# Performance work log

Measured on AMD Instinct MI355X. Metric: run time of the kernel, lower is better.

The kernel has to match this reference:

```python
import jax, jax.numpy as jnp
import numpy as np

H = 4          # num_heads (= num_kv_heads, num_kv_groups = 1)
DK = 256       # head_k_dim
DV = 256       # head_v_dim
M = 256        # num_slots
GATE_NORM = 16.0
EPS = 1e-5


def _rmsnorm(x, w):
    var = jnp.mean(jnp.square(x), axis=-1, keepdims=True)
    return x * jax.lax.rsqrt(var + EPS) * w


def _swish(x):
    return x * jax.nn.sigmoid(x)


def setup_inputs() -> dict:
    key = jax.random.key(0)
    ks = jax.random.split(key, 8)
    B, T, D = 4, 2048, 1024
    scale = 2 ** (-2.5) * (2.0 / (D + D)) ** 0.5 * (3.0 ** 0.5) * 2  # ~xavier*gain magnitude
    return {
        "hidden_states": jax.random.normal(ks[0], (B, T, D), jnp.float32),
        "norm_weight": jnp.ones((D,), jnp.float32),
        "w_q": jax.random.normal(ks[1], (D, D), jnp.float32) * scale,
        "w_k": jax.random.normal(ks[2], (D, D), jnp.float32) * scale,
        "w_v": jax.random.normal(ks[3], (D, D), jnp.float32) * scale,
        "w_f": jax.random.normal(ks[4], (H * M, D), jnp.float32) * scale,
        "gnorm_weight": jnp.ones((D,), jnp.float32),
        "w_o": jax.random.normal(ks[5], (D, D), jnp.float32) * scale,
    }


def _gsa_scan(q, k, v, s, g):
    # all inputs time-major: q [T,B,H,DK], k [T,B,H,DK], v [T,B,H,DV],
    # s [T,B,H,M] (slot write strength), g [T,B,H,M] (log forget gate)
    B, Hh = q.shape[1], q.shape[2]
    Hk0 = jnp.zeros((B, Hh, DK, M), q.dtype)
    Hv0 = jnp.zeros((B, Hh, M, DV), q.dtype)

    def step(carry, xs):
        Hk, Hv = carry
        qt, kt, vt, st, gt = xs
        lam = jnp.exp(gt)                                       # [B,H,M]
        # pass 1: linear attn over slots (gate on value/slot dim)
        Hk = Hk * lam[:, :, None, :] + kt[..., :, None] * st[..., None, :]
        z = jnp.einsum('bhk,bhkm->bhm', qt, Hk)                 # slot logits
        p = jax.nn.softmax(z, axis=-1)                          # slot read weights
        # pass 2: linear attn from slots to values (gate on key/slot dim)
        Hv = Hv * lam[..., :, None] + st[..., :, None] * vt[..., None, :]
        ot = jnp.einsum('bhm,bhmv->bhv', p, Hv)
        return (Hk, Hv), ot

    _, o = jax.lax.scan(step, (Hk0, Hv0), (q, k, v, s, g))
    return o  # [T,B,H,DV]


def reference(hidden_states, norm_weight, w_q, w_k, w_v, w_f, gnorm_weight, w_o):
    B, T, D = hidden_states.shape
    h = _rmsnorm(hidden_states, norm_weight)                    # norm_first
    q = _swish(h @ w_q.T).reshape(B, T, H, DK)                  # swish feature map
    k = _swish(h @ w_k.T).reshape(B, T, H, DK)
    v = _swish(h @ w_v.T).reshape(B, T, H, DV)
    f = jax.nn.log_sigmoid(h @ w_f.T).reshape(B, T, H, M) / GATE_NORM
    s = 1.0 - jnp.exp(f)
    tm = lambda x: jnp.transpose(x, (1, 0, 2, 3))               # [B,T,H,*] -> [T,B,H,*]
    o = _gsa_scan(tm(q), tm(k), tm(v), tm(s), tm(f))            # [T,B,H,DV]
    o = jnp.transpose(o, (1, 0, 2, 3)).reshape(B, T, H * DV)
    # use_norm & no output gate: swish -> RMSNorm -> o_proj
    o = _swish(o)
    o = _rmsnorm(o, gnorm_weight)
    return o @ w_o.T
```

## Files before the change

kernel.cpp:

```cpp
#include <hip/hip_runtime.h>
#include <hip/hip_bf16.h>

typedef unsigned short u16;
typedef unsigned int u32;

using bf16x8 = __bf16 __attribute__((ext_vector_type(8)));
using s16x8  = short  __attribute__((ext_vector_type(8)));
using f32x4  = float  __attribute__((ext_vector_type(4)));

#define DEV static __device__ __forceinline__

constexpr int T_ = 2048, D_ = 1024;
constexpr int C_ = 64, NC_ = 32;
constexpr float EPS_ = 1e-5f;

DEV float bf2f(u16 u) { return __uint_as_float(((u32)u) << 16); }
DEV u16 f2bf(float f) {
  u32 u = __float_as_uint(f);
  return (u16)((u + 0x7fffu + ((u >> 16) & 1u)) >> 16);
}
DEV float swishf(float x) { return x / (1.f + __expf(-x)); }
DEV f32x4 zero4() { f32x4 z = {0.f, 0.f, 0.f, 0.f}; return z; }

DEV bf16x8 ld8(const u16* p, int ld, int r0, int k0, int lane) {
  return *(const bf16x8*)(p + (size_t)(r0 + (lane & 15)) * ld +
                          (size_t)(k0 + ((lane >> 4) << 3)));
}
DEV f32x4 MFMA(bf16x8 a, bf16x8 b, f32x4 c) {
  return __builtin_amdgcn_mfma_f32_16x16x32_bf16(a, b, c, 0, 0, 0);
}
DEV void gld_lds16(const void* g, void* l) {
  __builtin_amdgcn_global_load_lds(
      (const __attribute__((address_space(1))) unsigned int*)g,
      (__attribute__((address_space(3))) unsigned int*)l, 16, 0, 0);
}

__global__ __launch_bounds__(256) void k_prep(
    const float* __restrict__ s0, const float* __restrict__ s1,
    const float* __restrict__ s2, const float* __restrict__ s3,
    const float* __restrict__ s4, u16* __restrict__ d0, u16* __restrict__ d1,
    u16* __restrict__ d2, u16* __restrict__ d3, u16* __restrict__ d4,
    const float* __restrict__ x, const float* __restrict__ w,
    u16* __restrict__ h) {
  const int bx = blockIdx.x, tid = threadIdx.x;
  if (bx < 5120) {
    const int wsel = bx >> 10;
    const float* s = (wsel == 0) ? s0 : (wsel == 1) ? s1 : (wsel == 2) ? s2
                     : (wsel == 3) ? s3 : s4;
    u16* d = (wsel == 0) ? d0 : (wsel == 1) ? d1 : (wsel == 2) ? d2
             : (wsel == 3) ? d3 : d4;
    const int i = (bx & 1023) * 256 + tid;
    float4 v = ((const float4*)s)[i];
    uint2 o;
    o.x = (u32)f2bf(v.x) | ((u32)f2bf(v.y) << 16);
    o.y = (u32)f2bf(v.z) | ((u32)f2bf(v.w) << 16);
    ((uint2*)d)[i] = o;
    return;
  }
  const int row = bx - 5120;
  float4 v = ((const float4*)(x + (size_t)row * D_))[tid];
  float ss = v.x * v.x + v.y * v.y + v.z * v.z + v.w * v.w;
#pragma unroll
  for (int d = 32; d >= 1; d >>= 1) ss += __shfl_xor(ss, d, 64);
  __shared__ float red[4];
  if ((tid & 63) == 0) red[tid >> 6] = ss;
  __syncthreads();
  float rs = rsqrtf((red[0] + red[1] + red[2] + red[3]) * (1.f / D_) + EPS_);
  float4 wv = ((const float4*)w)[tid];
  uint2 o;
  o.x = (u32)f2bf(v.x * rs * wv.x) | ((u32)f2bf(v.y * rs * wv.y) << 16);
  o.y = (u32)f2bf(v.z * rs * wv.z) | ((u32)f2bf(v.w * rs * wv.w) << 16);
  *(uint2*)(h + (size_t)row * D_ + tid * 4) = o;
}

__global__ __launch_bounds__(256) void k_swishnorm(const u16* __restrict__ x,
                                                   const float* __restrict__ w,
                                                   u16* __restrict__ o) {
  const int row = blockIdx.x, tid = threadIdx.x;
  uint2 pk = *(const uint2*)(x + (size_t)row * D_ + tid * 4);
  float v0 = swishf(bf2f((u16)(pk.x & 0xffff))), v1 = swishf(bf2f((u16)(pk.x >> 16)));
  float v2 = swishf(bf2f((u16)(pk.y & 0xffff))), v3 = swishf(bf2f((u16)(pk.y >> 16)));
  float ss = v0 * v0 + v1 * v1 + v2 * v2 + v3 * v3;
#pragma unroll
  for (int d = 32; d >= 1; d >>= 1) ss += __shfl_xor(ss, d, 64);
  __shared__ float red[4];
  if ((tid & 63) == 0) red[tid >> 6] = ss;
  __syncthreads();
  float rs = rsqrtf((red[0] + red[1] + red[2] + red[3]) * (1.f / D_) + EPS_);
  float4 wv = ((const float4*)w)[tid];
  uint2 ov;
  ov.x = (u32)f2bf(v0 * rs * wv.x) | ((u32)f2bf(v1 * rs * wv.y) << 16);
  ov.y = (u32)f2bf(v2 * rs * wv.z) | ((u32)f2bf(v3 * rs * wv.w) << 16);
  *(uint2*)(o + (size_t)row * D_ + tid * 4) = ov;
}

#define WAITV6() asm volatile("s_waitcnt vmcnt(6)" ::: "memory")
#define WAITV0() asm volatile("s_waitcnt vmcnt(0)" ::: "memory")
__global__ __launch_bounds__(256, 2) void k_gemm4(
    const u16* __restrict__ A, const u16* __restrict__ w0,
    const u16* __restrict__ w1, const u16* __restrict__ w2,
    const u16* __restrict__ w3, u16* __restrict__ oq, u16* __restrict__ okk,
    u16* __restrict__ ov, float* __restrict__ og) {
  __shared__ __align__(16) u16 As[3][128 * 32];
  __shared__ __align__(16) u16 Bs[3][4][64 * 32];
  const int m0 = blockIdx.x * 128, n0 = blockIdx.y * 64;
  const int tid = threadIdx.x, lane = tid & 63, wvi = tid >> 6;
  f32x4 acc[4][2][4];
#pragma unroll
  for (int w = 0; w < 4; w++)
#pragma unroll
    for (int i = 0; i < 2; i++)
#pragma unroll
      for (int j = 0; j < 4; j++) acc[w][i][j] = zero4();
  const int srow = tid >> 2, scb = (tid & 3) * 8;
  const u16* Ag = A + (size_t)(m0 + srow) * 1024 + scb;
  const u16* Wg0 = w0 + (size_t)(n0 + srow) * 1024 + scb;
  const u16* Wg1 = w1 + (size_t)(n0 + srow) * 1024 + scb;
  const u16* Wg2 = w2 + (size_t)(n0 + srow) * 1024 + scb;
  const u16* Wg3 = w3 + (size_t)(n0 + srow) * 1024 + scb;
  const int sofs = (wvi * 16) * 32;

  auto stage = [&](int buf, int kk) {
    gld_lds16(Ag + kk, &As[buf][sofs]);
    gld_lds16(Ag + kk + 64 * 1024, &As[buf][sofs + 64 * 32]);
    gld_lds16(Wg0 + kk, &Bs[buf][0][sofs]);
    gld_lds16(Wg1 + kk, &Bs[buf][1][sofs]);
    gld_lds16(Wg2 + kk, &Bs[buf][2][sofs]);
    gld_lds16(Wg3 + kk, &Bs[buf][3][sofs]);
  };
  auto compute = [&](int buf) {
    bf16x8 af[2];
#pragma unroll
    for (int i = 0; i < 2; i++)
      af[i] = ld8(As[buf], 32, wvi * 32 + 16 * i, 0, lane);
#pragma unroll
    for (int w = 0; w < 4; w++) {
      bf16x8 bfr[4];
#pragma unroll
      for (int j = 0; j < 4; j++) bfr[j] = ld8(Bs[buf][w], 32, 16 * j, 0, lane);
#pragma unroll
      for (int i = 0; i < 2; i++)
#pragma unroll
        for (int j = 0; j < 4; j++) acc[w][i][j] = MFMA(af[i], bfr[j], acc[w][i][j]);
    }
  };

  stage(0, 0);
  stage(1, 32);
  int b0 = 0, b1 = 1, b2 = 2;
  for (int t = 0; t < 32; ++t) {
    if (t < 31) { WAITV6(); } else { WAITV0(); }
    __builtin_amdgcn_sched_barrier(0);
    __builtin_amdgcn_s_barrier();
    __builtin_amdgcn_sched_barrier(0);
    if (t + 2 < 32) stage(b2, (t + 2) * 32);
    __builtin_amdgcn_s_setprio(1);
    compute(b0);
    __builtin_amdgcn_s_setprio(0);
    int tmp = b0; b0 = b1; b1 = b2; b2 = tmp;
  }
  const int q4 = lane >> 4, c15 = lane & 15;
#pragma unroll
  for (int w = 0; w < 4; w++)
#pragma unroll
    for (int i = 0; i < 2; i++)
#pragma unroll
      for (int j = 0; j < 4; j++)
#pragma unroll
        for (int r = 0; r < 4; r++) {
          int grow = m0 + wvi * 32 + 16 * i + 4 * q4 + r;
          int gcol = n0 + 16 * j + c15;
          size_t idx = (size_t)grow * 1024 + gcol;
          float val = acc[w][i][j][r];
          if (w < 3) {
            u16* o = (w == 0) ? oq : (w == 1) ? okk : ov;
            o[idx] = f2bf(swishf(val));
          } else {
            float g = (val >= 0.f) ? -log1pf(__expf(-val))
                                   : (val - log1pf(__expf(val)));
            og[idx] = g * (1.0f / 16.0f);
          }
        }
}

__global__ __launch_bounds__(256) void k_gemmO(const u16* __restrict__ A,
                                               const u16* __restrict__ W,
                                               float* __restrict__ ofin) {
  __shared__ __align__(16) u16 As[128 * 32];
  __shared__ __align__(16) u16 Bs[128 * 32];
  const int m0 = blockIdx.x * 128, n0 = blockIdx.y * 128;
  const int tid = threadIdx.x, lane = tid & 63, wvi = tid >> 6;
  const int wr = wvi >> 1, wc = wvi & 1;
  f32x4 acc[4][4];
#pragma unroll
  for (int i = 0; i < 4; i++)
#pragma unroll
    for (int j = 0; j < 4; j++) acc[i][j] = zero4();
  const int srow = tid >> 2, scb = (tid & 3) * 8;
  const u16* Ag = A + (size_t)(m0 + srow) * 1024 + scb;
  const u16* Wg = W + (size_t)(n0 + srow) * 1024 + scb;
  u16* AsW = As + (wvi * 16) * 32;
  u16* BsW = Bs + (wvi * 16) * 32;
  for (int kk = 0; kk < 1024; kk += 32) {
    gld_lds16(Ag + kk, AsW);
    gld_lds16(Ag + kk + 64 * 1024, AsW + 64 * 32);
    gld_lds16(Wg + kk, BsW);
    gld_lds16(Wg + kk + 64 * 1024, BsW + 64 * 32);
    __syncthreads();
    bf16x8 af[4], bfr[4];
#pragma unroll
    for (int i = 0; i < 4; i++) af[i] = ld8(As, 32, wr * 64 + 16 * i, 0, lane);
#pragma unroll
    for (int j = 0; j < 4; j++) bfr[j] = ld8(Bs, 32, wc * 64 + 16 * j, 0, lane);
#pragma unroll
    for (int i = 0; i < 4; i++)
#pragma unroll
      for (int j = 0; j < 4; j++) acc[i][j] = MFMA(af[i], bfr[j], acc[i][j]);
    __syncthreads();
  }
  const int q4 = lane >> 4, c15 = lane & 15;
#pragma unroll
  for (int i = 0; i < 4; i++)
#pragma unroll
    for (int j = 0; j < 4; j++)
#pragma unroll
      for (int r = 0; r < 4; r++) {
        int grow = m0 + wr * 64 + 16 * i + 4 * q4 + r;
        int gcol = n0 + wc * 64 + 16 * j + c15;
        ofin[(size_t)grow * 1024 + gcol] = acc[i][j][r];
      }
}

__global__ __launch_bounds__(256) void k_gates(float* __restrict__ g_inout,
                                               u16* __restrict__ U_t,
                                               float* __restrict__ Lam) {
  const int c = blockIdx.x, p = blockIdx.y, tid = threadIdx.x;
  const int b = p >> 2, hh = p & 3;
  const int R0 = b * T_ + c * C_, hb = hh * 256;
  float ga = 0.f, ea = 1.f;
  short ubuf[C_];
#pragma unroll
  for (int t = 0; t < C_; t++) {
    size_t gi = (size_t)(R0 + t) * D_ + hb + tid;
    float gv = g_inout[gi];
    ga += gv;
    ea = __expf(ga);
    ubuf[t] = (short)f2bf((1.f - __expf(gv)) * __expf(-ga));
    g_inout[gi] = ea;
  }
  Lam[((size_t)p * NC_ + c) * 256 + tid] = ea;
  u16* up = U_t + ((size_t)p * NC_ + c) * (256 * C_) + (size_t)tid * C_;
#pragma unroll
  for (int i = 0; i < 8; i++) {
    s16x8 w;
#pragma unroll
    for (int j = 0; j < 8; j++) w[j] = ubuf[i * 8 + j];
    *(s16x8*)(up + i * 8) = w;
  }
}

__global__ __launch_bounds__(256) void k_intra(
    const u16* __restrict__ kg, const u16* __restrict__ vg,
    const u16* __restrict__ U_t, const float* __restrict__ Lam,
    u16* __restrict__ Sk, u16* __restrict__ Sv) {
  __shared__ __align__(16) u16 KV[256 * 72];
  __shared__ float LamH[256];
  const int c = blockIdx.x, p = blockIdx.y;
  const int b = p >> 2, hh = p & 3;
  const int R0 = b * T_ + c * C_, hb = hh * 256;
  const int tid = threadIdx.x, lane = tid & 63, wvi = tid >> 6;
  const int q4 = lane >> 4, c15 = lane & 15;
  const size_t chunk = (size_t)p * NC_ + c;
  const u16* Uc = U_t + chunk * (256 * C_);
  const size_t scBase = chunk * (256 * 256);

  LamH[tid] = Lam[chunk * 256 + tid];
  for (int t = 0; t < C_; t++)
    KV[tid * 72 + t] = kg[(size_t)(R0 + t) * D_ + hb + tid];
  __syncthreads();

  for (int cb = 0; cb < 4; cb++) {
    f32x4 acc[4][4];
#pragma unroll
    for (int i = 0; i < 4; i++)
#pragma unroll
      for (int j = 0; j < 4; j++) acc[i][j] = zero4();
#pragma unroll
    for (int ks = 0; ks < 2; ks++) {
      bf16x8 af[4], bfr[4];
#pragma unroll
      for (int i = 0; i < 4; i++) af[i] = ld8(Uc, C_, 64 * wvi + 16 * i, 32 * ks, lane);
#pragma unroll
      for (int j = 0; j < 4; j++) bfr[j] = ld8(KV, 72, 64 * cb + 16 * j, 32 * ks, lane);
#pragma unroll
      for (int i = 0; i < 4; i++)
#pragma unroll
        for (int j = 0; j < 4; j++) acc[i][j] = MFMA(af[i], bfr[j], acc[i][j]);
    }
#pragma unroll
    for (int i = 0; i < 4; i++)
#pragma unroll
      for (int j = 0; j < 4; j++)
#pragma unroll
        for (int r = 0; r < 4; r++) {
          int ml = 64 * wvi + 16 * i + 4 * q4 + r;
          int dd = 64 * cb + 16 * j + c15;
          Sk[scBase + (size_t)ml * 256 + dd] = f2bf(acc[i][j][r] * LamH[ml]);
        }
  }
  __syncthreads();

  for (int t = 0; t < C_; t++)
    KV[tid * 72 + t] = vg[(size_t)(R0 + t) * D_ + hb + tid];
  __syncthreads();

  for (int cb = 0; cb < 4; cb++) {
    f32x4 acc[4][4];
#pragma unroll
    for (int i = 0; i < 4; i++)
#pragma unroll
      for (int j = 0; j < 4; j++) acc[i][j] = zero4();
#pragma unroll
    for (int ks = 0; ks < 2; ks++) {
      bf16x8 af[4], bfr[4];
#pragma unroll
      for (int i = 0; i < 4; i++) af[i] = ld8(KV, 72, 64 * wvi + 16 * i, 32 * ks, lane);
#pragma unroll
      for (int j = 0; j < 4; j++) bfr[j] = ld8(Uc, C_, 64 * cb + 16 * j, 32 * ks, lane);
#pragma unroll
      for (int i = 0; i < 4; i++)
#pragma unroll
        for (int j = 0; j < 4; j++) acc[i][j] = MFMA(af[i], bfr[j], acc[i][j]);
    }
#pragma unroll
    for (int i = 0; i < 4; i++)
#pragma unroll
      for (int j = 0; j < 4; j++)
#pragma unroll
        for (int r = 0; r < 4; r++) {
          int vv = 64 * wvi + 16 * i + 4 * q4 + r;
          int ml = 64 * cb + 16 * j + c15;
          Sv[scBase + (size_t)vv * 256 + ml] = f2bf(acc[i][j][r] * LamH[ml]);
        }
  }
}

__global__ __launch_bounds__(256) void k_scan(u16* __restrict__ Sk,
                                              u16* __restrict__ Sv,
                                              const float* __restrict__ Lam) {
  const int gid = blockIdx.x * 256 + threadIdx.x;
  const int st = gid >> 17;
  const int w = gid & 131071;
  const int p = w >> 13;
  const int r = (w >> 5) & 255;
  const int c0 = (w & 31) * 8;
  u16* S = st ? Sv : Sk;
  const size_t base = (size_t)p * NC_ * 65536 + (size_t)r * 256 + c0;
  const float* Lp = Lam + (size_t)p * NC_ * 256;
  float acc[8] = {0, 0, 0, 0, 0, 0, 0, 0};
  for (int c = 0; c < NC_; c++) {
    s16x8 in = *(const s16x8*)(S + base + (size_t)c * 65536);
    s16x8 ov;
#pragma unroll
    for (int j = 0; j < 8; j++) ov[j] = (short)f2bf(acc[j]);
    *(s16x8*)(S + base + (size_t)c * 65536) = ov;
    if (st == 0) {
      float lam = Lp[c * 256 + r];
#pragma unroll
      for (int j = 0; j < 8; j++) acc[j] = acc[j] * lam + bf2f((u16)in[j]);
    } else {
#pragma unroll
      for (int j = 0; j < 8; j++) {
        float lam = Lp[c * 256 + c0 + j];
        acc[j] = acc[j] * lam + bf2f((u16)in[j]);
      }
    }
  }
}

__global__ __launch_bounds__(256) void k_out(
    const u16* __restrict__ qg, const u16* __restrict__ kg,
    const u16* __restrict__ vg, const u16* __restrict__ U_t,
    const float* __restrict__ Eg, const u16* __restrict__ Sk,
    const u16* __restrict__ Sv, u16* __restrict__ orw) {
  __shared__ __align__(16) char lds[52224];
  u16* As = (u16*)lds;
  u16* Pt = (u16*)(lds + 9216);
  u16* UnH = (u16*)(lds + 43008);
  u16* VxH = (u16*)(lds + 43008);

  const int c = blockIdx.x, p = blockIdx.y;
  const int b = p >> 2, hh = p & 3;
  const int R0 = b * T_ + c * C_, hb = hh * 256;
  const int tid = threadIdx.x, lane = tid & 63, wvi = tid >> 6;
  const int q4 = lane >> 4, c15 = lane & 15;
  const u16* qbase = qg + (size_t)R0 * D_ + hb;
  const u16* kbase = kg + (size_t)R0 * D_ + hb;
  const float* Ebase = Eg + (size_t)R0 * D_ + hb;
  const size_t chunk = (size_t)p * NC_ + c;
  const u16* SkC = Sk + chunk * 65536;
  const u16* SvC = Sv + chunk * 65536;
  const u16* Uc = U_t + chunk * (256 * C_);

  {
    f32x4 acc[4];
#pragma unroll
    for (int n = 0; n < 4; n++) acc[n] = zero4();
#pragma unroll
    for (int ks = 0; ks < 8; ks++) {
      bf16x8 af = ld8(qbase, D_, 16 * wvi, 32 * ks, lane);
#pragma unroll
      for (int n = 0; n < 4; n++)
        acc[n] = MFMA(af, ld8(kbase, D_, 16 * n, 32 * ks, lane), acc[n]);
    }
#pragma unroll
    for (int n = 0; n < 4; n++)
#pragma unroll
      for (int r = 0; r < 4; r++) {
        int t = 16 * wvi + 4 * q4 + r, tau = 16 * n + c15;
        As[t * 72 + tau] = f2bf(tau <= t ? acc[n][r] : 0.f);
      }
  }
  __syncthreads();

  f32x4 zac[16];
#pragma unroll
  for (int mh = 0; mh < 2; mh++) {
#pragma unroll
    for (int n = 0; n < 8; n++) zac[mh * 8 + n] = zero4();
#pragma unroll
    for (int ks = 0; ks < 2; ks++) {
      bf16x8 af = ld8(As, 72, 16 * wvi, 32 * ks, lane);
#pragma unroll
      for (int n = 0; n < 8; n++)
        zac[mh * 8 + n] = MFMA(af, ld8(Uc, C_, mh * 128 + 16 * n, 32 * ks, lane),
                               zac[mh * 8 + n]);
    }
#pragma unroll
    for (int ks = 0; ks < 8; ks++) {
      bf16x8 af = ld8(qbase, D_, 16 * wvi, 32 * ks, lane);
#pragma unroll
      for (int n = 0; n < 8; n++)
        zac[mh * 8 + n] = MFMA(
            af, ld8(SkC + (size_t)mh * 128 * 256, 256, 16 * n, 32 * ks, lane),
            zac[mh * 8 + n]);
    }
#pragma unroll
    for (int n = 0; n < 8; n++)
#pragma unroll
      for (int r = 0; r < 4; r++) {
        int t = 16 * wvi + 4 * q4 + r;
        zac[mh * 8 + n][r] *= Ebase[(size_t)t * D_ + mh * 128 + 16 * n + c15];
      }
  }

  float invR[4];
#pragma unroll
  for (int r = 0; r < 4; r++) {
    float mx = -3.0e38f;
#pragma unroll
    for (int i = 0; i < 16; i++) mx = fmaxf(mx, zac[i][r]);
    mx = fmaxf(mx, __shfl_xor(mx, 1, 64));
    mx = fmaxf(mx, __shfl_xor(mx, 2, 64));
    mx = fmaxf(mx, __shfl_xor(mx, 4, 64));
    mx = fmaxf(mx, __shfl_xor(mx, 8, 64));
    float sm = 0.f;
#pragma unroll
    for (int i = 0; i < 16; i++) {
      float e = __expf(zac[i][r] - mx);
      zac[i][r] = e;
      sm += e;
    }
    sm += __shfl_xor(sm, 1, 64);
    sm += __shfl_xor(sm, 2, 64);
    sm += __shfl_xor(sm, 4, 64);
    sm += __shfl_xor(sm, 8, 64);
    invR[r] = 1.f / sm;
  }
#pragma unroll
  for (int i = 0; i < 16; i++)
#pragma unroll
    for (int r = 0; r < 4; r++) {
      int t = 16 * wvi + 4 * q4 + r;
      int m = (i >> 3) * 128 + 16 * (i & 7) + c15;
      float e = Ebase[(size_t)t * D_ + m];
      Pt[t * 264 + m] = f2bf(zac[i][r] * invR[r] * e);
    }
  __syncthreads();

  {
    f32x4 wac[4];
#pragma unroll
    for (int n = 0; n < 4; n++) wac[n] = zero4();
    for (int mq = 0; mq < 4; mq++) {
      {
        int mloc = tid >> 2, th = tid & 3;
        const u16* ur = Uc + (size_t)(mq * 64 + mloc) * C_ + th * 16;
#pragma unroll
        for (int tt = 0; tt < 2; tt++) {
          s16x8 v = *(const s16x8*)(ur + tt * 8);
#pragma unroll
          for (int j = 0; j < 8; j++)
            UnH[(th * 16 + tt * 8 + j) * 72 + mloc] = (u16)v[j];
        }
      }
      __syncthreads();
#pragma unroll
      for (int ks = 0; ks < 2; ks++) {
        bf16x8 af = ld8(Pt, 264, 16 * wvi, mq * 64 + 32 * ks, lane);
#pragma unroll
        for (int n = 0; n < 4; n++)
          wac[n] = MFMA(af, ld8(UnH, 72, 16 * n, 32 * ks, lane), wac[n]);
      }
      __syncthreads();
    }
#pragma unroll
    for (int n = 0; n < 4; n++)
#pragma unroll
      for (int r = 0; r < 4; r++) {
        int t = 16 * wvi + 4 * q4 + r, tau = 16 * n + c15;
        As[t * 72 + tau] = f2bf(tau <= t ? wac[n][r] : 0.f);
      }
  }
  __syncthreads();

  for (int vq = 0; vq < 4; vq++) {
    {
      int vloc = tid >> 2, th = tid & 3;
#pragma unroll 4
      for (int tt = 0; tt < 16; tt++) {
        int t = th * 16 + tt;
        VxH[vloc * 72 + t] = vg[(size_t)(R0 + t) * D_ + hb + vq * 64 + vloc];
      }
    }
    __syncthreads();
    f32x4 oac[4];
#pragma unroll
    for (int n = 0; n < 4; n++) oac[n] = zero4();
#pragma unroll
    for (int ks = 0; ks < 8; ks++) {
      bf16x8 af = ld8(Pt, 264, 16 * wvi, 32 * ks, lane);
#pragma unroll
      for (int n = 0; n < 4; n++)
        oac[n] = MFMA(af, ld8(SvC + (size_t)vq * 64 * 256, 256, 16 * n, 32 * ks, lane), oac[n]);
    }
#pragma unroll
    for (int ks = 0; ks < 2; ks++) {
      bf16x8 af = ld8(As, 72, 16 * wvi, 32 * ks, lane);
#pragma unroll
      for (int n = 0; n < 4; n++)
        oac[n] = MFMA(af, ld8(VxH, 72, 16 * n, 32 * ks, lane), oac[n]);
    }
#pragma unroll
    for (int n = 0; n < 4; n++)
#pragma unroll
      for (int r = 0; r < 4; r++) {
        int t = 16 * wvi + 4 * q4 + r;
        int vc = vq * 64 + 16 * n + c15;
        orw[(size_t)(R0 + t) * D_ + hb + vc] = f2bf(oac[n][r]);
      }
    __syncthreads();
  }
}

extern "C" void kernel_launch(void* const* d_in, const int* in_sizes, int n_in,
                              void* d_out, int out_size, void* d_ws, size_t ws_size,
                              hipStream_t stream) {
  (void)in_sizes; (void)n_in; (void)out_size; (void)ws_size;
  const float* x   = (const float*)d_in[0];
  const float* nw  = (const float*)d_in[1];
  const float* wq  = (const float*)d_in[2];
  const float* wk  = (const float*)d_in[3];
  const float* wvp = (const float*)d_in[4];
  const float* wf  = (const float*)d_in[5];
  const float* gw  = (const float*)d_in[6];
  const float* wo  = (const float*)d_in[7];
  float* out = (float*)d_out;
  char* ws = (char*)d_ws;
  const size_t MB = 1024ull * 1024ull;
  u16*   hbuf = (u16*)(ws);
  u16*   qb   = (u16*)(ws + 16 * MB);
  u16*   kb   = (u16*)(ws + 32 * MB);
  u16*   vb   = (u16*)(ws + 48 * MB);
  float* gb   = (float*)(ws + 64 * MB);
  u16*   SkB  = (u16*)(ws + 96 * MB);
  u16*   SvB  = (u16*)(ws + 160 * MB);
  float* Lam  = (float*)(ws + 224 * MB);
  u16*   orw  = (u16*)(ws + 226 * MB);
  u16*   wqb  = (u16*)(ws + 242 * MB);
  u16*   wkb  = (u16*)(ws + 244 * MB);
  u16*   wvb  = (u16*)(ws + 246 * MB);
  u16*   wfb  = (u16*)(ws + 248 * MB);
  u16*   wob  = (u16*)(ws + 250 * MB);
  u16*   U_t  = hbuf;

  k_prep<<<dim3(13312), dim3(256), 0, stream>>>(
      wq, wk, wvp, wf, wo, wqb, wkb, wvb, wfb, wob, x, nw, hbuf);
  k_gemm4<<<dim3(64, 16), dim3(256), 0, stream>>>(
      hbuf, wqb, wkb, wvb, wfb, qb, kb, vb, gb);
  k_gates<<<dim3(NC_, 16), dim3(256), 0, stream>>>(gb, U_t, Lam);
  k_intra<<<dim3(NC_, 16), dim3(256), 0, stream>>>(kb, vb, U_t, Lam, SkB, SvB);
  k_scan<<<dim3(1024), dim3(256), 0, stream>>>(SkB, SvB, Lam);
  k_out<<<dim3(NC_, 16), dim3(256), 0, stream>>>(qb, kb, vb, U_t, gb, SkB, SvB, orw);
  k_swishnorm<<<dim3(8192), dim3(256), 0, stream>>>(orw, gw, hbuf);
  k_gemmO<<<dim3(64, 8), dim3(256), 0, stream>>>(hbuf, wob, out);
}
```

Baseline: 478.3 us.

## Stage chunk state tiles through LDS in k_out instead of per-wave global loads

Before this change, every wave in k_out loaded the per-chunk Sk and Sv state matrices straight from global memory as MFMA B fragments, so all four waves fetched the same data. The kernel now copies each 64x256 quarter of Sk and Sv into a padded LDS buffer with coalesced 16-byte loads and reads the MFMA operands from LDS. The q fragments are hoisted into registers and reused across the four slot quarters. This needs more LDS (76.8KB per block), which may lower occupancy, and adds extra barriers.

```diff
diff --git a/kernel.cpp b/kernel.cpp
--- a/kernel.cpp
+++ b/kernel.cpp
@@ -383,9 +383,10 @@
     const u16* __restrict__ vg, const u16* __restrict__ U_t,
     const float* __restrict__ Eg, const u16* __restrict__ Sk,
     const u16* __restrict__ Sv, u16* __restrict__ orw) {
-  __shared__ __align__(16) char lds[52224];
-  u16* As = (u16*)lds;
-  u16* Pt = (u16*)(lds + 9216);
+  __shared__ __align__(16) char lds[76800];
+  u16* As  = (u16*)lds;
+  u16* Pt  = (u16*)(lds + 9216);
+  u16* Sst = (u16*)(lds + 43008);
   u16* UnH = (u16*)(lds + 43008);
   u16* VxH = (u16*)(lds + 43008);
 
@@ -402,6 +403,16 @@
   const u16* SvC = Sv + chunk * 65536;
   const u16* Uc = U_t + chunk * (256 * C_);
 
+  auto stageQ = [&](const u16* src) {
+#pragma unroll
+    for (int j = 0; j < 8; j++) {
+      int byte = j * 4096 + tid * 16;
+      int rr = byte >> 9, cb = byte & 511;
+      s16x8 v = *(const s16x8*)((const char*)src + byte);
+      *(s16x8*)((char*)Sst + rr * 528 + cb) = v;
+    }
+  };
+
   {
     f32x4 acc[4];
 #pragma unroll
@@ -423,36 +434,39 @@
   }
   __syncthreads();
 
+  bf16x8 qf[8];
+#pragma unroll
+  for (int ks = 0; ks < 8; ks++) qf[ks] = ld8(qbase, D_, 16 * wvi, 32 * ks, lane);
   f32x4 zac[16];
 #pragma unroll
-  for (int mh = 0; mh < 2; mh++) {
-#pragma unroll
-    for (int n = 0; n < 8; n++) zac[mh * 8 + n] = zero4();
-#pragma unroll
-    for (int ks = 0; ks < 2; ks++) {
-      bf16x8 af = ld8(As, 72, 16 * wvi, 32 * ks, lane);
-#pragma unroll
-      for (int n = 0; n < 8; n++)
-        zac[mh * 8 + n] = MFMA(af, ld8(Uc, C_, mh * 128 + 16 * n, 32 * ks, lane),
-                               zac[mh * 8 + n]);
-    }
-#pragma unroll
-    for (int ks = 0; ks < 8; ks++) {
-      bf16x8 af = ld8(qbase, D_, 16 * wvi, 32 * ks, lane);
-#pragma unroll
-      for (int n = 0; n < 8; n++)
-        zac[mh * 8 + n] = MFMA(
-            af, ld8(SkC + (size_t)mh * 128 * 256, 256, 16 * n, 32 * ks, lane),
-            zac[mh * 8 + n]);
-    }
-#pragma unroll
-    for (int n = 0; n < 8; n++)
-#pragma unroll
-      for (int r = 0; r < 4; r++) {
-        int t = 16 * wvi + 4 * q4 + r;
-        zac[mh * 8 + n][r] *= Ebase[(size_t)t * D_ + mh * 128 + 16 * n + c15];
-      }
-  }
+  for (int i = 0; i < 16; i++) zac[i] = zero4();
+#pragma unroll
+  for (int ks = 0; ks < 2; ks++) {
+    bf16x8 af = ld8(As, 72, 16 * wvi, 32 * ks, lane);
+#pragma unroll
+    for (int i = 0; i < 16; i++)
+      zac[i] = MFMA(af, ld8(Uc, C_, (i >> 3) * 128 + 16 * (i & 7), 32 * ks, lane),
+                    zac[i]);
+  }
+  for (int mq = 0; mq < 4; mq++) {
+    stageQ(SkC + (size_t)mq * 64 * 256);
+    __syncthreads();
+#pragma unroll
+    for (int ks = 0; ks < 8; ks++)
+#pragma unroll
+      for (int nl = 0; nl < 4; nl++) {
+        int zi = (mq >> 1) * 8 + (mq & 1) * 4 + nl;
+        zac[zi] = MFMA(qf[ks], ld8(Sst, 264, 16 * nl, 32 * ks, lane), zac[zi]);
+      }
+    __syncthreads();
+  }
+#pragma unroll
+  for (int i = 0; i < 16; i++)
+#pragma unroll
+    for (int r = 0; r < 4; r++) {
+      int t = 16 * wvi + 4 * q4 + r;
+      zac[i][r] *= Ebase[(size_t)t * D_ + (i >> 3) * 128 + 16 * (i & 7) + c15];
+    }
 
   float invR[4];
 #pragma unroll
@@ -525,6 +539,19 @@
   __syncthreads();
 
   for (int vq = 0; vq < 4; vq++) {
+    stageQ(SvC + (size_t)vq * 64 * 256);
+    __syncthreads();
+    f32x4 oac[4];
+#pragma unroll
+    for (int n = 0; n < 4; n++) oac[n] = zero4();
+#pragma unroll
+    for (int ks = 0; ks < 8; ks++) {
+      bf16x8 af = ld8(Pt, 264, 16 * wvi, 32 * ks, lane);
+#pragma unroll
+      for (int n = 0; n < 4; n++)
+        oac[n] = MFMA(af, ld8(Sst, 264, 16 * n, 32 * ks, lane), oac[n]);
+    }
+    __syncthreads();
     {
       int vloc = tid >> 2, th = tid & 3;
 #pragma unroll 4
@@ -534,16 +561,6 @@
       }
     }
     __syncthreads();
-    f32x4 oac[4];
-#pragma unroll
-    for (int n = 0; n < 4; n++) oac[n] = zero4();
-#pragma unroll
-    for (int ks = 0; ks < 8; ks++) {
-      bf16x8 af = ld8(Pt, 264, 16 * wvi, 32 * ks, lane);
-#pragma unroll
-      for (int n = 0; n < 4; n++)
-        oac[n] = MFMA(af, ld8(SvC + (size_t)vq * 64 * 256, 256, 16 * n, 32 * ks, lane), oac[n]);
-    }
 #pragma unroll
     for (int ks = 0; ks < 2; ks++) {
       bf16x8 af = ld8(As, 72, 16 * wvi, 32 * ks, lane);
```

New measurement: 456.5 us. 4.5% less time.
